# Optimization experiments

Measured on AMD Instinct MI355X. Metric: run time of the kernel, lower is better.

Reference implementation:

```python
import jax, jax.numpy as jnp
import numpy as np

HIDDEN = 1024
NUM_HEADS = 16
HEAD_DIM = HIDDEN // NUM_HEADS  # 64
B, LQ, LK = 2, 2048, 2048


def setup_inputs() -> dict:
    key = jax.random.key(0)
    ks = jax.random.split(key, 9)
    s = 1.0 / np.sqrt(HIDDEN)
    return {
        "hidden_states_query": jax.random.normal(ks[0], (B, LQ, HIDDEN), jnp.float32),
        "hidden_states_key": jax.random.normal(ks[1], (B, LK, HIDDEN), jnp.float32),
        "attention_mask": jnp.ones((B, LQ, LK), jnp.float32),
        "Wq": jax.random.normal(ks[2], (HIDDEN, HIDDEN), jnp.float32) * s,
        "bq": jax.random.normal(ks[3], (HIDDEN,), jnp.float32) * s,
        "Wk": jax.random.normal(ks[4], (HIDDEN, HIDDEN), jnp.float32) * s,
        "bk": jax.random.normal(ks[5], (HIDDEN,), jnp.float32) * s,
        "Wv": jax.random.normal(ks[6], (HIDDEN, HIDDEN), jnp.float32) * s,
        "bv": jax.random.normal(ks[7], (HIDDEN,), jnp.float32) * s,
    }


def _split_heads(x):
    # [B, L, H*D] -> [B, nH, L, D]
    b, l, _ = x.shape
    return x.reshape(b, l, NUM_HEADS, HEAD_DIM).transpose(0, 2, 1, 3)


def reference(hidden_states_query, hidden_states_key, attention_mask, Wq, bq, Wk, bk, Wv, bv):
    # nn.Linear applies x @ W.T + b; weights here stored as [out, in]
    q = _split_heads(hidden_states_query @ Wq.T + bq)
    k = _split_heads(hidden_states_key @ Wk.T + bk)
    v = _split_heads(hidden_states_key @ Wv.T + bv)
    scale = 1.0 / np.sqrt(HEAD_DIM)
    scores = jnp.einsum("bhqd,bhkd->bhqk", q * scale, k)  # [B, nH, Lq, Lk]
    # mask: 1 -> 0, 0 -> -10000, broadcast over heads
    scores = scores + ((1.0 - attention_mask) * -10000.0)[:, None, :, :]
    probs = jax.nn.softmax(scores, axis=-1)
    ctx = jnp.einsum("bhqk,bhkd->bhqd", probs, v)
    b, h, lq, d = ctx.shape
    return ctx.transpose(0, 2, 1, 3).reshape(b, lq, h * d)
```

## Files before the change

### kernel.cpp

```cpp
#include <hip/hip_runtime.h>
#include <hip/hip_bf16.h>

#define HID 1024
#define NH 16
#define HD 64
#define SEQ 2048
#define NB 2
#define NTOK (NB * SEQ)

typedef __attribute__((ext_vector_type(8))) short bf16x8;
typedef __attribute__((ext_vector_type(4))) float f32x4;
typedef __attribute__((ext_vector_type(4))) unsigned u32x4;

#define QSCALE 0.18033688011112042f
#define MASKSCALE 1.4426950408889634f

#define MFMA16(a, b, c) __builtin_amdgcn_mfma_f32_16x16x32_bf16((a), (b), (c), 0, 0, 0)

__device__ __forceinline__ unsigned short f2bf(float f) {
    unsigned u = __builtin_bit_cast(unsigned, f);
    u += 0x7FFFu + ((u >> 16) & 1u);
    return (unsigned short)(u >> 16);
}
__device__ __forceinline__ unsigned cvtpk(float a, float b) {
    unsigned r;
    asm("v_cvt_pk_bf16_f32 %0, %1, %2" : "=v"(r) : "v"(a), "v"(b));
    return r;
}
__device__ __forceinline__ void gload_lds16(const unsigned short* g, unsigned short* l) {
    __builtin_amdgcn_global_load_lds(
        (const __attribute__((address_space(1))) unsigned int*)g,
        (__attribute__((address_space(3))) unsigned int*)l, 16, 0, 0);
}

__global__ __launch_bounds__(256) void cvt_all(
    const float* __restrict__ xq, const float* __restrict__ xk,
    const float* __restrict__ Wq, const float* __restrict__ Wk, const float* __restrict__ Wv,
    const float* __restrict__ mask,
    unsigned short* __restrict__ dxq, unsigned short* __restrict__ dxk,
    unsigned short* __restrict__ dwq, unsigned short* __restrict__ dwk,
    unsigned short* __restrict__ dwv, int* __restrict__ flags) {
    const int id = blockIdx.x;
    if (id >= 11264) {
        const int lane = threadIdx.x & 63;
        int i = ((id - 11264) * 256 + threadIdx.x) * 4;
        float4 v = *(const float4*)(mask + i);
        bool ok = (v.x == 1.0f) && (v.y == 1.0f) && (v.z == 1.0f) && (v.w == 1.0f);
        unsigned long long bal = __ballot(ok);
        int g = lane >> 4;
        if ((lane & 15) == 0) {
            unsigned m16 = (unsigned)(bal >> (g * 16)) & 0xFFFFu;
            if (m16 != 0xFFFFu) {
                int b = i >> 22;
                int rem = i & 4194303;
                int q = rem >> 11, k = rem & 2047;
                atomicAnd(&flags[(b << 10) + ((q >> 6) << 5) + (k >> 6)], 0);
            }
        }
        return;
    }
    const float* src;
    unsigned short* dst;
    int base;
    float scale = 1.0f;
    if (id < 4096)       { src = xq; dst = dxq; base = 0; }
    else if (id < 8192)  { src = xk; dst = dxk; base = 4096; }
    else if (id < 9216)  { src = Wq; dst = dwq; base = 8192; scale = QSCALE; }
    else if (id < 10240) { src = Wk; dst = dwk; base = 9216; }
    else                 { src = Wv; dst = dwv; base = 10240; }
    int i = ((id - base) * 256 + threadIdx.x) * 4;
    float4 v = *(const float4*)(src + i);
    ushort4 o;
    o.x = f2bf(v.x * scale); o.y = f2bf(v.y * scale);
    o.z = f2bf(v.z * scale); o.w = f2bf(v.w * scale);
    *(ushort4*)(dst + i) = o;
}

__global__ __launch_bounds__(256, 3) void proj_gemm(
    const unsigned short* __restrict__ xq, const unsigned short* __restrict__ xk,
    const unsigned short* __restrict__ wq, const unsigned short* __restrict__ wk,
    const unsigned short* __restrict__ wv,
    const float* __restrict__ bq, const float* __restrict__ bk, const float* __restrict__ bv,
    unsigned short* __restrict__ Qh, unsigned short* __restrict__ Kh,
    unsigned short* __restrict__ Vt) {
    __shared__ __align__(16) unsigned short As[3][128 * 32];
    __shared__ __align__(16) unsigned short Bs[3][128 * 32];

    const int id = blockIdx.x;
    const int xid = (id & 7) * 96 + (id >> 3);
    const unsigned short *A, *B;
    const float* bias;
    float bsc = 1.0f;
    unsigned short* out;
    int mt, nt;
    bool tr = false;
    if (xid < 256)      { A = xq; B = wq; bias = bq; bsc = QSCALE; out = Qh;
                          mt = xid >> 3; nt = xid & 7; }
    else if (xid < 512) { A = xk; B = wk; bias = bk; out = Kh;
                          mt = (xid - 256) >> 3; nt = (xid - 256) & 7; }
    else                { A = wv; B = xk; bias = bv; out = Vt; tr = true;
                          mt = (xid - 512) & 7; nt = (xid - 512) >> 3; }
    const int m0 = mt * 128, n0 = nt * 128;
    const int tid = threadIdx.x, wave = tid >> 6, lane = tid & 63;
    const int wr = (wave >> 1) * 64, wc = (wave & 1) * 64;
    const int fr = lane & 15, hi = lane >> 4;

    const int uswz = (hi ^ ((fr >> 1) & 3)) << 3;
    const int abase = (wr + fr) * 32 + uswz;
    const int bbase = (wc + fr) * 32 + uswz;

    const int srow = wave * 16 + (lane >> 2);
    const int sunit = (lane & 3) ^ ((lane >> 3) & 3);
    const unsigned short* Asrc = A + (size_t)(m0 + srow) * HID + sunit * 8;
    const unsigned short* Bsrc = B + (size_t)(n0 + srow) * HID + sunit * 8;

    unsigned short *cA = As[0], *nA = As[1], *fA = As[2];
    unsigned short *cB = Bs[0], *nB = Bs[1], *fB = Bs[2];

    f32x4 acc[4][4] = {};

#define PSTG(t, ap, bp)                                                          \
    do {                                                                         \
        gload_lds16(Asrc + (t) * 32, (ap) + wave * 512);                         \
        gload_lds16(Asrc + (size_t)64 * HID + (t) * 32, (ap) + 2048 + wave * 512); \
        gload_lds16(Bsrc + (t) * 32, (bp) + wave * 512);                         \
        gload_lds16(Bsrc + (size_t)64 * HID + (t) * 32, (bp) + 2048 + wave * 512); \
    } while (0)

    PSTG(0, cA, cB);
    PSTG(1, nA, nB);

    for (int t = 0; t < 32; ++t) {
        if (t < 31) asm volatile("s_waitcnt vmcnt(4)" ::: "memory");
        else        asm volatile("s_waitcnt vmcnt(0)" ::: "memory");
        __builtin_amdgcn_s_barrier();
        if (t < 30) PSTG(t + 2, fA, fB);

        bf16x8 af[4], bfr[4];
#pragma unroll
        for (int i = 0; i < 4; ++i) af[i] = *(const bf16x8*)&cA[abase + i * 512];
#pragma unroll
        for (int j = 0; j < 4; ++j) bfr[j] = *(const bf16x8*)&cB[bbase + j * 512];
        __builtin_amdgcn_s_setprio(1);
#pragma unroll
        for (int i = 0; i < 4; ++i)
#pragma unroll
            for (int j = 0; j < 4; ++j)
                acc[i][j] = MFMA16(af[i], bfr[j], acc[i][j]);
        __builtin_amdgcn_s_setprio(0);

        unsigned short* ta = cA; cA = nA; nA = fA; fA = ta;
        unsigned short* tb = cB; cB = nB; nB = fB; fB = tb;
    }
#undef PSTG

#pragma unroll
    for (int i = 0; i < 4; ++i)
#pragma unroll
        for (int j = 0; j < 4; ++j)
#pragma unroll
            for (int r = 0; r < 4; ++r) {
                int row = m0 + wr + i * 16 + hi * 4 + r;
                int col = n0 + wc + j * 16 + fr;
                float v = acc[i][j][r];
                if (!tr) {
                    v += bsc * bias[col];
                    int b = row >> 11, l = row & 2047, hh = col >> 6, d = col & 63;
                    out[(((size_t)(b * NH + hh)) * SEQ + l) * HD + d] = f2bf(v);
                } else {
                    v += bias[row];
                    int b = col >> 11, ll = col & 2047, hh = row >> 6, d = row & 63;
                    int lp = (ll & ~0x1C) | ((ll & 0x0C) << 1) | ((ll & 0x10) >> 2);
                    out[(((size_t)(b * NH + hh)) * HD + d) * SEQ + lp] = f2bf(v);
                }
            }
}

__global__ __launch_bounds__(256, 3) void flash_attn(
    const unsigned short* __restrict__ Qh, const unsigned short* __restrict__ Kh,
    const unsigned short* __restrict__ Vt, const float* __restrict__ mask,
    const int* __restrict__ flags, float* __restrict__ out) {
    __shared__ __align__(16) unsigned short Ks[3][64 * 64];
    __shared__ __align__(16) unsigned short Vs[3][64 * 64];

    const int tid = threadIdx.x, wave = tid >> 6, lane = tid & 63;
    const int id = blockIdx.x;
    const int bh = (id & 7) * 4 + ((id >> 3) & 3);
    const int qi = id >> 5;
    const int b = bh >> 4, h = bh & 15;
    const size_t hoff = (size_t)bh * SEQ * HD;
    const int fr = lane & 15, hi = lane >> 4;
    const int f7 = fr & 7, swz3 = f7 << 3;
    const int qa = qi * 64 + wave * 16 + fr;

    bf16x8 qfa0 = *(const bf16x8*)&Qh[hoff + (size_t)qa * HD + hi * 8];
    bf16x8 qfa1 = *(const bf16x8*)&Qh[hoff + (size_t)qa * HD + 32 + hi * 8];

    const float* mrowA = mask + (size_t)b * SEQ * SEQ + (size_t)qa * SEQ;
    const int* frow = flags + (b << 10) + (qi << 5);
    int fv = frow[lane & 31];
    const unsigned long long bm = __ballot(fv != 0);

    const int srow = wave * 8 + (lane >> 3);
    const int sch = (lane & 7) ^ (srow & 7);
    const unsigned short* kbase = Kh + hoff + (size_t)srow * HD + (sch << 3);
    const unsigned short* vbase = Vt + hoff + (size_t)srow * SEQ + (sch << 3);

    f32x4 accA[4] = {};
    f32x4 laccA = {};
    const bf16x8 ones = {0x3F80, 0x3F80, 0x3F80, 0x3F80, 0x3F80, 0x3F80, 0x3F80, 0x3F80};

    unsigned short *cK = &Ks[0][0], *nK = &Ks[1][0], *fK = &Ks[2][0];
    unsigned short *cV = &Vs[0][0], *nV = &Vs[1][0], *fV = &Vs[2][0];

#define STG(t, kd, vd)                                                           \
    do {                                                                         \
        gload_lds16(kbase + (size_t)(t) * 64 * HD, (kd) + (wave * 8) * 64);      \
        gload_lds16(kbase + (size_t)((t) * 64 + 32) * HD, (kd) + (wave * 8 + 32) * 64); \
        gload_lds16(vbase + (t) * 64, (vd) + (wave * 8) * 64);                   \
        gload_lds16(vbase + (size_t)32 * SEQ + (t) * 64, (vd) + (wave * 8 + 32) * 64); \
    } while (0)

    STG(0, cK, cV);
    STG(1, nK, nV);

    for (int t = 0; t < 32; ++t) {
        if (t < 31) asm volatile("s_waitcnt vmcnt(4)" ::: "memory");
        else        asm volatile("s_waitcnt vmcnt(0)" ::: "memory");
        __builtin_amdgcn_s_barrier();
        if (t < 30) STG(t + 2, fK, fV);

        f32x4 sA[4];
        __builtin_amdgcn_s_setprio(1);
#pragma unroll
        for (int sub = 0; sub < 4; ++sub) {
            const int rbase = (sub * 16 + fr) * 64;
            bf16x8 kf0 = *(const bf16x8*)&cK[rbase + ((hi << 3) ^ swz3)];
            bf16x8 kf1 = *(const bf16x8*)&cK[rbase + (((hi + 4) << 3) ^ swz3)];
            f32x4 z = {0.f, 0.f, 0.f, 0.f};
            z = MFMA16(kf0, qfa0, z);
            z = MFMA16(kf1, qfa1, z);
            sA[sub] = z;
        }
        __builtin_amdgcn_s_setprio(0);

        if (!((bm >> t) & 1)) {
            const int k0 = t * 64;
#pragma unroll
            for (int sub = 0; sub < 4; ++sub) {
                float4 ma = *(const float4*)&mrowA[k0 + sub * 16 + hi * 4];
                sA[sub][0] += (1.f - ma.x) * (-10000.f * MASKSCALE);
                sA[sub][1] += (1.f - ma.y) * (-10000.f * MASKSCALE);
                sA[sub][2] += (1.f - ma.z) * (-10000.f * MASKSCALE);
                sA[sub][3] += (1.f - ma.w) * (-10000.f * MASKSCALE);
            }
        }

#pragma unroll
        for (int sub = 0; sub < 4; ++sub)
#pragma unroll
            for (int r = 0; r < 4; ++r)
                sA[sub][r] = __builtin_amdgcn_exp2f(sA[sub][r]);

        u32x4 w0, w1;
        w0[0] = cvtpk(sA[0][0], sA[0][1]); w0[1] = cvtpk(sA[0][2], sA[0][3]);
        w0[2] = cvtpk(sA[1][0], sA[1][1]); w0[3] = cvtpk(sA[1][2], sA[1][3]);
        w1[0] = cvtpk(sA[2][0], sA[2][1]); w1[1] = cvtpk(sA[2][2], sA[2][3]);
        w1[2] = cvtpk(sA[3][0], sA[3][1]); w1[3] = cvtpk(sA[3][2], sA[3][3]);
        bf16x8 pA0 = __builtin_bit_cast(bf16x8, w0);
        bf16x8 pA1 = __builtin_bit_cast(bf16x8, w1);

        __builtin_amdgcn_s_setprio(1);
        laccA = MFMA16(ones, pA0, laccA);
        laccA = MFMA16(ones, pA1, laccA);

#pragma unroll
        for (int sub = 0; sub < 4; ++sub) {
            const int rbase = (sub * 16 + fr) * 64;
            bf16x8 vf0 = *(const bf16x8*)&cV[rbase + ((hi << 3) ^ swz3)];
            bf16x8 vf1 = *(const bf16x8*)&cV[rbase + (((hi + 4) << 3) ^ swz3)];
            accA[sub] = MFMA16(vf0, pA0, accA[sub]);
            accA[sub] = MFMA16(vf1, pA1, accA[sub]);
        }
        __builtin_amdgcn_s_setprio(0);

        unsigned short* tk = cK; cK = nK; nK = fK; fK = tk;
        unsigned short* tv = cV; cV = nV; nV = fV; fV = tv;
    }
#undef STG

    float rA = 1.0f / laccA[0];
#pragma unroll
    for (int sub = 0; sub < 4; ++sub) {
        float4 oA = {accA[sub][0] * rA, accA[sub][1] * rA, accA[sub][2] * rA, accA[sub][3] * rA};
        *(float4*)&out[((size_t)b * SEQ + qa) * HID + h * HD + sub * 16 + hi * 4] = oA;
    }
}

extern "C" void kernel_launch(void* const* d_in, const int* in_sizes, int n_in,
                              void* d_out, int out_size, void* d_ws, size_t ws_size,
                              hipStream_t stream) {
    const float* xq = (const float*)d_in[0];
    const float* xk = (const float*)d_in[1];
    const float* mask = (const float*)d_in[2];
    const float* Wq = (const float*)d_in[3];
    const float* bq = (const float*)d_in[4];
    const float* Wk = (const float*)d_in[5];
    const float* bk = (const float*)d_in[6];
    const float* Wv = (const float*)d_in[7];
    const float* bv = (const float*)d_in[8];
    float* out = (float*)d_out;

    const size_t NX = (size_t)NTOK * HID;
    const size_t NW = (size_t)HID * HID;
    const size_t need = (5 * NX + 3 * NW) * sizeof(unsigned short) + 2048 * sizeof(int);
    if (ws_size < need) return;

    unsigned short* ws = (unsigned short*)d_ws;
    unsigned short* xq_b = ws;
    unsigned short* xk_b = xq_b + NX;
    unsigned short* wq_b = xk_b + NX;
    unsigned short* wk_b = wq_b + NW;
    unsigned short* wv_b = wk_b + NW;
    unsigned short* Qh = wv_b + NW;
    unsigned short* Kh = Qh + NX;
    unsigned short* Vt = Kh + NX;
    int* flags = (int*)(Vt + NX);

    hipMemsetAsync(flags, 0xFF, 2048 * sizeof(int), stream);
    cvt_all<<<19456, 256, 0, stream>>>(xq, xk, Wq, Wk, Wv, mask,
                                       xq_b, xk_b, wq_b, wk_b, wv_b, flags);
    proj_gemm<<<768, 256, 0, stream>>>(xq_b, xk_b, wq_b, wk_b, wv_b,
                                       bq, bk, bv, Qh, Kh, Vt);
    flash_attn<<<1024, 256, 0, stream>>>(Qh, Kh, Vt, mask, flags, out);
}
```

Baseline: 112.6 us.

## Process two 16-row query tiles per wave to reuse K/V LDS fragments

```diff
diff --git a/kernel.cpp b/kernel.cpp
--- a/kernel.cpp
+++ b/kernel.cpp
@@ -176,7 +176,7 @@
             }
 }
 
-__global__ __launch_bounds__(256, 3) void flash_attn(
+__global__ __launch_bounds__(256, 2) void flash_attn(
     const unsigned short* __restrict__ Qh, const unsigned short* __restrict__ Kh,
     const unsigned short* __restrict__ Vt, const float* __restrict__ mask,
     const int* __restrict__ flags, float* __restrict__ out) {
@@ -191,13 +191,17 @@
     const size_t hoff = (size_t)bh * SEQ * HD;
     const int fr = lane & 15, hi = lane >> 4;
     const int f7 = fr & 7, swz3 = f7 << 3;
-    const int qa = qi * 64 + wave * 16 + fr;
+    const int qa = qi * 128 + wave * 32 + fr;
+    const int qb = qa + 16;
 
     bf16x8 qfa0 = *(const bf16x8*)&Qh[hoff + (size_t)qa * HD + hi * 8];
     bf16x8 qfa1 = *(const bf16x8*)&Qh[hoff + (size_t)qa * HD + 32 + hi * 8];
+    bf16x8 qfb0 = *(const bf16x8*)&Qh[hoff + (size_t)qb * HD + hi * 8];
+    bf16x8 qfb1 = *(const bf16x8*)&Qh[hoff + (size_t)qb * HD + 32 + hi * 8];
 
     const float* mrowA = mask + (size_t)b * SEQ * SEQ + (size_t)qa * SEQ;
-    const int* frow = flags + (b << 10) + (qi << 5);
+    const float* mrowB = mask + (size_t)b * SEQ * SEQ + (size_t)qb * SEQ;
+    const int* frow = flags + (b << 10) + ((qi * 2 + (wave >> 1)) << 5);
     int fv = frow[lane & 31];
     const unsigned long long bm = __ballot(fv != 0);
 
@@ -206,8 +210,8 @@
     const unsigned short* kbase = Kh + hoff + (size_t)srow * HD + (sch << 3);
     const unsigned short* vbase = Vt + hoff + (size_t)srow * SEQ + (sch << 3);
 
-    f32x4 accA[4] = {};
-    f32x4 laccA = {};
+    f32x4 accA[4] = {}, accB[4] = {};
+    f32x4 laccA = {}, laccB = {};
     const bf16x8 ones = {0x3F80, 0x3F80, 0x3F80, 0x3F80, 0x3F80, 0x3F80, 0x3F80, 0x3F80};
 
     unsigned short *cK = &Ks[0][0], *nK = &Ks[1][0], *fK = &Ks[2][0];
@@ -230,7 +234,7 @@
         __builtin_amdgcn_s_barrier();
         if (t < 30) STG(t + 2, fK, fV);
 
-        f32x4 sA[4];
+        f32x4 sA[4], sB[4];
         __builtin_amdgcn_s_setprio(1);
 #pragma unroll
         for (int sub = 0; sub < 4; ++sub) {
@@ -241,6 +245,10 @@
             z = MFMA16(kf0, qfa0, z);
             z = MFMA16(kf1, qfa1, z);
             sA[sub] = z;
+            f32x4 w = {0.f, 0.f, 0.f, 0.f};
+            w = MFMA16(kf0, qfb0, w);
+            w = MFMA16(kf1, qfb1, w);
+            sB[sub] = w;
         }
         __builtin_amdgcn_s_setprio(0);
 
@@ -253,26 +261,41 @@
                 sA[sub][1] += (1.f - ma.y) * (-10000.f * MASKSCALE);
                 sA[sub][2] += (1.f - ma.z) * (-10000.f * MASKSCALE);
                 sA[sub][3] += (1.f - ma.w) * (-10000.f * MASKSCALE);
+                float4 mv = *(const float4*)&mrowB[k0 + sub * 16 + hi * 4];
+                sB[sub][0] += (1.f - mv.x) * (-10000.f * MASKSCALE);
+                sB[sub][1] += (1.f - mv.y) * (-10000.f * MASKSCALE);
+                sB[sub][2] += (1.f - mv.z) * (-10000.f * MASKSCALE);
+                sB[sub][3] += (1.f - mv.w) * (-10000.f * MASKSCALE);
             }
         }
 
 #pragma unroll
         for (int sub = 0; sub < 4; ++sub)
 #pragma unroll
-            for (int r = 0; r < 4; ++r)
+            for (int r = 0; r < 4; ++r) {
                 sA[sub][r] = __builtin_amdgcn_exp2f(sA[sub][r]);
-
-        u32x4 w0, w1;
-        w0[0] = cvtpk(sA[0][0], sA[0][1]); w0[1] = cvtpk(sA[0][2], sA[0][3]);
-        w0[2] = cvtpk(sA[1][0], sA[1][1]); w0[3] = cvtpk(sA[1][2], sA[1][3]);
-        w1[0] = cvtpk(sA[2][0], sA[2][1]); w1[1] = cvtpk(sA[2][2], sA[2][3]);
-        w1[2] = cvtpk(sA[3][0], sA[3][1]); w1[3] = cvtpk(sA[3][2], sA[3][3]);
-        bf16x8 pA0 = __builtin_bit_cast(bf16x8, w0);
-        bf16x8 pA1 = __builtin_bit_cast(bf16x8, w1);
+                sB[sub][r] = __builtin_amdgcn_exp2f(sB[sub][r]);
+            }
+
+        u32x4 wa0, wa1, wb0, wb1;
+        wa0[0] = cvtpk(sA[0][0], sA[0][1]); wa0[1] = cvtpk(sA[0][2], sA[0][3]);
+        wa0[2] = cvtpk(sA[1][0], sA[1][1]); wa0[3] = cvtpk(sA[1][2], sA[1][3]);
+        wa1[0] = cvtpk(sA[2][0], sA[2][1]); wa1[1] = cvtpk(sA[2][2], sA[2][3]);
+        wa1[2] = cvtpk(sA[3][0], sA[3][1]); wa1[3] = cvtpk(sA[3][2], sA[3][3]);
+        wb0[0] = cvtpk(sB[0][0], sB[0][1]); wb0[1] = cvtpk(sB[0][2], sB[0][3]);
+        wb0[2] = cvtpk(sB[1][0], sB[1][1]); wb0[3] = cvtpk(sB[1][2], sB[1][3]);
+        wb1[0] = cvtpk(sB[2][0], sB[2][1]); wb1[1] = cvtpk(sB[2][2], sB[2][3]);
+        wb1[2] = cvtpk(sB[3][0], sB[3][1]); wb1[3] = cvtpk(sB[3][2], sB[3][3]);
+        bf16x8 pA0 = __builtin_bit_cast(bf16x8, wa0);
+        bf16x8 pA1 = __builtin_bit_cast(bf16x8, wa1);
+        bf16x8 pB0 = __builtin_bit_cast(bf16x8, wb0);
+        bf16x8 pB1 = __builtin_bit_cast(bf16x8, wb1);
 
         __builtin_amdgcn_s_setprio(1);
         laccA = MFMA16(ones, pA0, laccA);
         laccA = MFMA16(ones, pA1, laccA);
+        laccB = MFMA16(ones, pB0, laccB);
+        laccB = MFMA16(ones, pB1, laccB);
 
 #pragma unroll
         for (int sub = 0; sub < 4; ++sub) {
@@ -281,6 +304,8 @@
             bf16x8 vf1 = *(const bf16x8*)&cV[rbase + (((hi + 4) << 3) ^ swz3)];
             accA[sub] = MFMA16(vf0, pA0, accA[sub]);
             accA[sub] = MFMA16(vf1, pA1, accA[sub]);
+            accB[sub] = MFMA16(vf0, pB0, accB[sub]);
+            accB[sub] = MFMA16(vf1, pB1, accB[sub]);
         }
         __builtin_amdgcn_s_setprio(0);
 
@@ -289,11 +314,13 @@
     }
 #undef STG
 
-    float rA = 1.0f / laccA[0];
+    float rA = 1.0f / laccA[0], rB = 1.0f / laccB[0];
 #pragma unroll
     for (int sub = 0; sub < 4; ++sub) {
         float4 oA = {accA[sub][0] * rA, accA[sub][1] * rA, accA[sub][2] * rA, accA[sub][3] * rA};
         *(float4*)&out[((size_t)b * SEQ + qa) * HID + h * HD + sub * 16 + hi * 4] = oA;
+        float4 oB = {accB[sub][0] * rB, accB[sub][1] * rB, accB[sub][2] * rB, accB[sub][3] * rB};
+        *(float4*)&out[((size_t)b * SEQ + qb) * HID + h * HD + sub * 16 + hi * 4] = oB;
     }
 }
 
@@ -332,5 +359,5 @@
                                        xq_b, xk_b, wq_b, wk_b, wv_b, flags);
     proj_gemm<<<768, 256, 0, stream>>>(xq_b, xk_b, wq_b, wk_b, wv_b,
                                        bq, bk, bv, Qh, Kh, Vt);
-    flash_attn<<<1024, 256, 0, stream>>>(Qh, Kh, Vt, mask, flags, out);
-}
+    flash_attn<<<512, 256, 0, stream>>>(Qh, Kh, Vt, mask, flags, out);
+}
```

After: 105.7 us. 6.2% less time.

## Split KV across waves with 128-query blocks and cross-wave LDS reduction

Applied to the files above, without the earlier changes.

```diff
diff --git a/kernel.cpp b/kernel.cpp
--- a/kernel.cpp
+++ b/kernel.cpp
@@ -170,18 +170,16 @@
                 } else {
                     v += bias[row];
                     int b = col >> 11, ll = col & 2047, hh = row >> 6, d = row & 63;
-                    int lp = (ll & ~0x1C) | ((ll & 0x0C) << 1) | ((ll & 0x10) >> 2);
-                    out[(((size_t)(b * NH + hh)) * HD + d) * SEQ + lp] = f2bf(v);
+                    out[(((size_t)(b * NH + hh)) * HD + d) * SEQ + ll] = f2bf(v);
                 }
             }
 }
 
-__global__ __launch_bounds__(256, 3) void flash_attn(
+__global__ __launch_bounds__(256, 2) void flash_attn(
     const unsigned short* __restrict__ Qh, const unsigned short* __restrict__ Kh,
     const unsigned short* __restrict__ Vt, const float* __restrict__ mask,
     const int* __restrict__ flags, float* __restrict__ out) {
-    __shared__ __align__(16) unsigned short Ks[3][64 * 64];
-    __shared__ __align__(16) unsigned short Vs[3][64 * 64];
+    __shared__ __align__(16) unsigned short LB[8][64 * 64];
 
     const int tid = threadIdx.x, wave = tid >> 6, lane = tid & 63;
     const int id = blockIdx.x;
@@ -190,110 +188,161 @@
     const int b = bh >> 4, h = bh & 15;
     const size_t hoff = (size_t)bh * SEQ * HD;
     const int fr = lane & 15, hi = lane >> 4;
-    const int f7 = fr & 7, swz3 = f7 << 3;
-    const int qa = qi * 64 + wave * 16 + fr;
-
-    bf16x8 qfa0 = *(const bf16x8*)&Qh[hoff + (size_t)qa * HD + hi * 8];
-    bf16x8 qfa1 = *(const bf16x8*)&Qh[hoff + (size_t)qa * HD + 32 + hi * 8];
-
-    const float* mrowA = mask + (size_t)b * SEQ * SEQ + (size_t)qa * SEQ;
-    const int* frow = flags + (b << 10) + (qi << 5);
-    int fv = frow[lane & 31];
-    const unsigned long long bm = __ballot(fv != 0);
+    const int f7 = fr & 7;
+
+    bf16x8 qf0[8], qf1[8];
+#pragma unroll
+    for (int qs = 0; qs < 8; ++qs) {
+        const size_t qrow = hoff + (size_t)(qi * 128 + qs * 16 + fr) * HD;
+        qf0[qs] = *(const bf16x8*)&Qh[qrow + hi * 8];
+        qf1[qs] = *(const bf16x8*)&Qh[qrow + 32 + hi * 8];
+    }
+
+    const float* mbase = mask + (size_t)b * SEQ * SEQ;
+    const int* fr0 = flags + (b << 10) + ((qi * 2) << 5);
+    const int* fr1 = flags + (b << 10) + ((qi * 2 + 1) << 5);
+    int fv0 = fr0[lane & 31], fv1 = fr1[lane & 31];
+    const unsigned long long bm0 = __ballot(fv0 != 0);
+    const unsigned long long bm1 = __ballot(fv1 != 0);
 
     const int srow = wave * 8 + (lane >> 3);
     const int sch = (lane & 7) ^ (srow & 7);
     const unsigned short* kbase = Kh + hoff + (size_t)srow * HD + (sch << 3);
     const unsigned short* vbase = Vt + hoff + (size_t)srow * SEQ + (sch << 3);
 
-    f32x4 accA[4] = {};
-    f32x4 laccA = {};
-    const bf16x8 ones = {0x3F80, 0x3F80, 0x3F80, 0x3F80, 0x3F80, 0x3F80, 0x3F80, 0x3F80};
-
-    unsigned short *cK = &Ks[0][0], *nK = &Ks[1][0], *fK = &Ks[2][0];
-    unsigned short *cV = &Vs[0][0], *nV = &Vs[1][0], *fV = &Vs[2][0];
-
-#define STG(t, kd, vd)                                                           \
-    do {                                                                         \
-        gload_lds16(kbase + (size_t)(t) * 64 * HD, (kd) + (wave * 8) * 64);      \
-        gload_lds16(kbase + (size_t)((t) * 64 + 32) * HD, (kd) + (wave * 8 + 32) * 64); \
-        gload_lds16(vbase + (t) * 64, (vd) + (wave * 8) * 64);                   \
-        gload_lds16(vbase + (size_t)32 * SEQ + (t) * 64, (vd) + (wave * 8 + 32) * 64); \
+    f32x4 acc[8][4] = {};
+    float lp[8] = {};
+
+    const int krow = (wave * 16 + fr) * 64;
+    const int ku0 = ((hi) ^ f7) << 3;
+    const int ku1 = ((4 + hi) ^ f7) << 3;
+    const int vu = (((wave * 2 + (hi >> 1)) ^ f7) << 3) + ((hi & 1) << 2);
+
+#define STG(t, ki, vi)                                                                \
+    do {                                                                              \
+        gload_lds16(kbase + (size_t)(t) * 64 * HD, LB[ki] + (wave * 8) * 64);         \
+        gload_lds16(kbase + (size_t)((t) * 64 + 32) * HD, LB[ki] + (wave * 8 + 32) * 64); \
+        gload_lds16(vbase + (t) * 64, LB[vi] + (wave * 8) * 64);                      \
+        gload_lds16(vbase + (size_t)32 * SEQ + (t) * 64, LB[vi] + (wave * 8 + 32) * 64); \
     } while (0)
 
-    STG(0, cK, cV);
-    STG(1, nK, nV);
-
-    for (int t = 0; t < 32; ++t) {
-        if (t < 31) asm volatile("s_waitcnt vmcnt(4)" ::: "memory");
-        else        asm volatile("s_waitcnt vmcnt(0)" ::: "memory");
-        __builtin_amdgcn_s_barrier();
-        if (t < 30) STG(t + 2, fK, fV);
-
-        f32x4 sA[4];
-        __builtin_amdgcn_s_setprio(1);
-#pragma unroll
-        for (int sub = 0; sub < 4; ++sub) {
-            const int rbase = (sub * 16 + fr) * 64;
-            bf16x8 kf0 = *(const bf16x8*)&cK[rbase + ((hi << 3) ^ swz3)];
-            bf16x8 kf1 = *(const bf16x8*)&cK[rbase + (((hi + 4) << 3) ^ swz3)];
-            f32x4 z = {0.f, 0.f, 0.f, 0.f};
-            z = MFMA16(kf0, qfa0, z);
-            z = MFMA16(kf1, qfa1, z);
-            sA[sub] = z;
+#define FPAIR(kA, vA, kB, vB, tt)                                                     \
+    do {                                                                              \
+        bf16x8 ka0 = *(const bf16x8*)&LB[kA][krow + ku0];                             \
+        bf16x8 ka1 = *(const bf16x8*)&LB[kA][krow + ku1];                             \
+        bf16x8 kb0 = *(const bf16x8*)&LB[kB][krow + ku0];                             \
+        bf16x8 kb1 = *(const bf16x8*)&LB[kB][krow + ku1];                             \
+        bf16x8 vf[4];                                                                 \
+        _Pragma("unroll")                                                             \
+        for (int ds = 0; ds < 4; ++ds) {                                              \
+            const int off = (ds * 16 + fr) * 64 + vu;                                 \
+            uint2 va = *(const uint2*)&LB[vA][off];                                   \
+            uint2 vb = *(const uint2*)&LB[vB][off];                                   \
+            u32x4 vv = {va.x, va.y, vb.x, vb.y};                                      \
+            vf[ds] = __builtin_bit_cast(bf16x8, vv);                                  \
+        }                                                                             \
+        _Pragma("unroll")                                                             \
+        for (int qs = 0; qs < 8; ++qs) {                                              \
+            f32x4 st = {0.f, 0.f, 0.f, 0.f}, su = {0.f, 0.f, 0.f, 0.f};               \
+            __builtin_amdgcn_s_setprio(1);                                            \
+            st = MFMA16(ka0, qf0[qs], st);                                            \
+            st = MFMA16(ka1, qf1[qs], st);                                            \
+            su = MFMA16(kb0, qf0[qs], su);                                            \
+            su = MFMA16(kb1, qf1[qs], su);                                            \
+            __builtin_amdgcn_s_setprio(0);                                            \
+            const unsigned long long bms = (qs < 4) ? bm0 : bm1;                      \
+            if (!((bms >> (tt)) & 1) || !((bms >> ((tt) + 1)) & 1)) {                 \
+                const int qq = qi * 128 + qs * 16 + fr;                               \
+                const float* mrow = mbase + (size_t)qq * SEQ + wave * 16 + hi * 4;    \
+                float4 ma = *(const float4*)&mrow[(tt) * 64];                         \
+                float4 mbv = *(const float4*)&mrow[((tt) + 1) * 64];                  \
+                st[0] += (1.f - ma.x) * (-10000.f * MASKSCALE);                       \
+                st[1] += (1.f - ma.y) * (-10000.f * MASKSCALE);                       \
+                st[2] += (1.f - ma.z) * (-10000.f * MASKSCALE);                       \
+                st[3] += (1.f - ma.w) * (-10000.f * MASKSCALE);                       \
+                su[0] += (1.f - mbv.x) * (-10000.f * MASKSCALE);                      \
+                su[1] += (1.f - mbv.y) * (-10000.f * MASKSCALE);                      \
+                su[2] += (1.f - mbv.z) * (-10000.f * MASKSCALE);                      \
+                su[3] += (1.f - mbv.w) * (-10000.f * MASKSCALE);                      \
+            }                                                                         \
+            _Pragma("unroll")                                                         \
+            for (int r = 0; r < 4; ++r) {                                             \
+                st[r] = __builtin_amdgcn_exp2f(st[r]);                                \
+                su[r] = __builtin_amdgcn_exp2f(su[r]);                                \
+            }                                                                         \
+            lp[qs] += ((st[0] + st[1]) + (st[2] + st[3])) +                           \
+                      ((su[0] + su[1]) + (su[2] + su[3]));                            \
+            u32x4 pw = {cvtpk(st[0], st[1]), cvtpk(st[2], st[3]),                     \
+                        cvtpk(su[0], su[1]), cvtpk(su[2], su[3])};                    \
+            bf16x8 pb = __builtin_bit_cast(bf16x8, pw);                               \
+            __builtin_amdgcn_s_setprio(1);                                            \
+            _Pragma("unroll")                                                         \
+            for (int ds = 0; ds < 4; ++ds)                                            \
+                acc[qs][ds] = MFMA16(vf[ds], pb, acc[qs][ds]);                        \
+            __builtin_amdgcn_s_setprio(0);                                            \
+        }                                                                             \
+    } while (0)
+
+    STG(0, 0, 4);
+    STG(1, 1, 5);
+
+    for (int ii = 0; ii < 8; ++ii) {
+        const int t0 = ii * 4;
+        asm volatile("s_waitcnt vmcnt(0)" ::: "memory");
+        __builtin_amdgcn_s_barrier();
+        STG(t0 + 2, 2, 6);
+        STG(t0 + 3, 3, 7);
+        FPAIR(0, 4, 1, 5, t0);
+        asm volatile("s_waitcnt vmcnt(0)" ::: "memory");
+        __builtin_amdgcn_s_barrier();
+        if (ii < 7) {
+            STG(t0 + 4, 0, 4);
+            STG(t0 + 5, 1, 5);
         }
-        __builtin_amdgcn_s_setprio(0);
-
-        if (!((bm >> t) & 1)) {
-            const int k0 = t * 64;
-#pragma unroll
-            for (int sub = 0; sub < 4; ++sub) {
-                float4 ma = *(const float4*)&mrowA[k0 + sub * 16 + hi * 4];
-                sA[sub][0] += (1.f - ma.x) * (-10000.f * MASKSCALE);
-                sA[sub][1] += (1.f - ma.y) * (-10000.f * MASKSCALE);
-                sA[sub][2] += (1.f - ma.z) * (-10000.f * MASKSCALE);
-                sA[sub][3] += (1.f - ma.w) * (-10000.f * MASKSCALE);
+        FPAIR(2, 6, 3, 7, t0 + 2);
+    }
+#undef STG
+#undef FPAIR
+
+    __builtin_amdgcn_s_barrier();
+    float* R = (float*)&LB[0][0];
+#pragma unroll
+    for (int hf = 0; hf < 2; ++hf) {
+        if (wave >= 1) {
+            const int wb = (wave - 1) * 4352;
+#pragma unroll
+            for (int qs2 = 0; qs2 < 4; ++qs2) {
+                const int qs = hf * 4 + qs2;
+#pragma unroll
+                for (int ds = 0; ds < 4; ++ds)
+                    *(f32x4*)&R[wb + (qs2 * 4 + ds) * 256 + lane * 4] = acc[qs][ds];
+                R[wb + 4096 + qs2 * 64 + lane] = lp[qs];
             }
         }
-
-#pragma unroll
-        for (int sub = 0; sub < 4; ++sub)
-#pragma unroll
-            for (int r = 0; r < 4; ++r)
-                sA[sub][r] = __builtin_amdgcn_exp2f(sA[sub][r]);
-
-        u32x4 w0, w1;
-        w0[0] = cvtpk(sA[0][0], sA[0][1]); w0[1] = cvtpk(sA[0][2], sA[0][3]);
-        w0[2] = cvtpk(sA[1][0], sA[1][1]); w0[3] = cvtpk(sA[1][2], sA[1][3]);
-        w1[0] = cvtpk(sA[2][0], sA[2][1]); w1[1] = cvtpk(sA[2][2], sA[2][3]);
-        w1[2] = cvtpk(sA[3][0], sA[3][1]); w1[3] = cvtpk(sA[3][2], sA[3][3]);
-        bf16x8 pA0 = __builtin_bit_cast(bf16x8, w0);
-        bf16x8 pA1 = __builtin_bit_cast(bf16x8, w1);
-
-        __builtin_amdgcn_s_setprio(1);
-        laccA = MFMA16(ones, pA0, laccA);
-        laccA = MFMA16(ones, pA1, laccA);
-
-#pragma unroll
-        for (int sub = 0; sub < 4; ++sub) {
-            const int rbase = (sub * 16 + fr) * 64;
-            bf16x8 vf0 = *(const bf16x8*)&cV[rbase + ((hi << 3) ^ swz3)];
-            bf16x8 vf1 = *(const bf16x8*)&cV[rbase + (((hi + 4) << 3) ^ swz3)];
-            accA[sub] = MFMA16(vf0, pA0, accA[sub]);
-            accA[sub] = MFMA16(vf1, pA1, accA[sub]);
+        __builtin_amdgcn_s_barrier();
+        if (wave == 0) {
+#pragma unroll
+            for (int qs2 = 0; qs2 < 4; ++qs2) {
+                const int qs = hf * 4 + qs2;
+                float ls = lp[qs];
+#pragma unroll
+                for (int w = 0; w < 3; ++w) ls += R[w * 4352 + 4096 + qs2 * 64 + lane];
+                ls += __shfl_xor(ls, 16);
+                ls += __shfl_xor(ls, 32);
+                const float rinv = 1.0f / ls;
+                const int qq = qi * 128 + qs * 16 + fr;
+#pragma unroll
+                for (int ds = 0; ds < 4; ++ds) {
+                    f32x4 a = acc[qs][ds];
+#pragma unroll
+                    for (int w = 0; w < 3; ++w)
+                        a += *(const f32x4*)&R[w * 4352 + (qs2 * 4 + ds) * 256 + lane * 4];
+                    float4 o = {a[0] * rinv, a[1] * rinv, a[2] * rinv, a[3] * rinv};
+                    *(float4*)&out[((size_t)b * SEQ + qq) * HID + h * HD + ds * 16 + hi * 4] = o;
+                }
+            }
         }
-        __builtin_amdgcn_s_setprio(0);
-
-        unsigned short* tk = cK; cK = nK; nK = fK; fK = tk;
-        unsigned short* tv = cV; cV = nV; nV = fV; fV = tv;
-    }
-#undef STG
-
-    float rA = 1.0f / laccA[0];
-#pragma unroll
-    for (int sub = 0; sub < 4; ++sub) {
-        float4 oA = {accA[sub][0] * rA, accA[sub][1] * rA, accA[sub][2] * rA, accA[sub][3] * rA};
-        *(float4*)&out[((size_t)b * SEQ + qa) * HID + h * HD + sub * 16 + hi * 4] = oA;
+        __builtin_amdgcn_s_barrier();
     }
 }
 
@@ -332,5 +381,5 @@
                                        xq_b, xk_b, wq_b, wk_b, wv_b, flags);
     proj_gemm<<<768, 256, 0, stream>>>(xq_b, xk_b, wq_b, wk_b, wv_b,
                                        bq, bk, bv, Qh, Kh, Vt);
-    flash_attn<<<1024, 256, 0, stream>>>(Qh, Kh, Vt, mask, flags, out);
-}
+    flash_attn<<<512, 256, 0, stream>>>(Qh, Kh, Vt, mask, flags, out);
+}
```

Measured after the change: 271.9 us. 2.41x slower.
